# Kernel tuning notes

Hardware: AMD Instinct MI355X
Metric: run time of the kernel (lower is better)

The kernel has to match this reference:

```python
import jax, jax.numpy as jnp
import numpy as np

B, C, H, W, K = 2, 36, 512, 512, 9
GROUPS, GSIZE = 3, 12  # channel groups 0:12, 12:24, 24:36


def _grid_sample_bilinear(feat, gx, gy):
    """Bilinear grid_sample, align_corners=True. feat [B,C,H,W]; gx,gy [B,H,W] in [-1,1]."""
    Bn, Cn, Hn, Wn = feat.shape
    px = (gx + 1.0) * 0.5 * (Wn - 1)
    py = (gy + 1.0) * 0.5 * (Hn - 1)
    x0 = jnp.floor(px)
    y0 = jnp.floor(py)
    wx = (px - x0)[:, None, :, :]
    wy = (py - y0)[:, None, :, :]
    x0i = jnp.clip(x0.astype(jnp.int32), 0, Wn - 1)
    x1i = jnp.clip(x0i + 1, 0, Wn - 1)
    y0i = jnp.clip(y0.astype(jnp.int32), 0, Hn - 1)
    y1i = jnpip = jnp.clip(y0.astype(jnp.int32) + 1, 0, Hn - 1)
    flat = feat.reshape(Bn, Cn, Hn * Wn)
    gather = jax.vmap(lambda f, yi, xi: f[:, yi * Wn + xi])  # -> [B,C,H,W]
    v00 = gather(flat, y0i, x0i)
    v01 = gather(flat, y0i, x1i)
    v10 = gather(flat, y1i, x0i)
    v11 = gather(flat, y1i, x1i)
    return (v00 * (1 - wx) * (1 - wy) + v01 * wx * (1 - wy)
            + v10 * (1 - wx) * wy + v11 * wx * wy)


def setup_inputs() -> dict:
    key = jax.random.key(0)
    k1, k2, k3 = jax.random.split(key, 3)
    features = jax.random.normal(k1, (B, C, H, W), jnp.float32)
    offset_x = jax.random.normal(k2, (B, K, H, W), jnp.float32) * 16.0
    offset_y = jax.random.normal(k3, (B, K, H, W), jnp.float32) * 16.0
    left_x = jnp.broadcast_to(jnp.arange(W, dtype=jnp.float32)[None, None, None, :], (B, 1, H, W))
    left_y = jnp.broadcast_to(jnp.arange(H, dtype=jnp.float32)[None, None, :, None], (B, 1, H, W))
    return {"features": features, "offset_x": offset_x, "offset_y": offset_y,
            "left_x": jnp.array(left_x), "left_y": jnp.array(left_y)}


def reference(features, offset_x, offset_y, left_x, left_y):
    Hn, Wn = features.shape[2], features.shape[3]
    # clamp candidate coords to image, then normalize to [-1,1]
    rx = jnp.clip(left_x + offset_x, 0.0, Wn - 1)
    ry = jnp.clip(left_y + offset_y, 0.0, Hn - 1)
    gx = (rx - (Wn - 1) / 2.0) / ((Wn - 1) / 2.0)  # [B,K,H,W]
    gy = (ry - (Hn - 1) / 2.0) / ((Hn - 1) / 2.0)

    def per_candidate(g):
        gxk, gyk = g  # each [B,H,W]
        a = _grid_sample_bilinear(features, gxk, gyk)  # [B,36,H,W]
        a2 = jnp.roll(a, 12, axis=1)
        a3 = jnp.roll(a, 24, axis=1)

        def grp_mean(d):  # [B,36,H,W] -> [B,3,H,W] mean over 12-channel groups
            return d.reshape(d.shape[0], GROUPS, GSIZE, d.shape[2], d.shape[3]).mean(axis=2)

        s = jnp.concatenate([grp_mean(-jnp.abs(features - a)),
                             grp_mean(-jnp.abs(features - a2)),
                             grp_mean(-jnp.abs(features - a3))], axis=1)  # [B,9,H,W]
        return jnp.max(s, axis=1)  # top-1 of sort == max  -> [B,H,W]

    strengths = jax.lax.map(per_candidate,
                            (jnp.moveaxis(gx, 1, 0), jnp.moveaxis(gy, 1, 0)))  # [K,B,H,W]
    strengths = jnp.moveaxis(strengths, 0, 1)  # [B,K,H,W]

    wgt = jax.nn.softmax(strengths * 1000.0, axis=1)
    ox = jnp.sum(offset_x * wgt, axis=1, keepdims=True)
    oy = jnp.sum(offset_y * wgt, axis=1, keepdims=True)
    oy = jnp.clip(oy + left_y, 0.0, Hn - 1) - left_y
    ox = jnp.clip(ox + left_x, 0.0, Wn - 1) - left_x
    return ox, oy
```

## Files before the change

kernel.cpp:

```cpp
#include <hip/hip_runtime.h>
#include <math.h>

#define B_ 2
#define C_ 36
#define H_ 512
#define W_ 512
#define K_ 9
#define HW_ (H_ * W_)
#define ROWF4 (W_ * C_ / 4)

__global__ __launch_bounds__(256) void transpose_kernel(const float* __restrict__ in,
                                                        float* __restrict__ out) {
  __shared__ float tile[64][37];
  int blk = blockIdx.x;
  int wt = blk & 7;
  int h = (blk >> 3) & (H_ - 1);
  int b = blk >> 12;
  int w0 = wt << 6;
  int tid = threadIdx.x;
  const float* src = in + ((size_t)b * C_) * HW_ + (size_t)h * W_ + w0;
#pragma unroll
  for (int it = 0; it < 9; ++it) {
    int idx = it * 256 + tid;
    int c = idx >> 6;
    int wl = idx & 63;
    tile[wl][c] = src[(size_t)c * HW_ + wl];
  }
  __syncthreads();
  float* dst = out + (((size_t)b * H_ + h) * W_ + w0) * C_;
#pragma unroll
  for (int it = 0; it < 9; ++it) {
    int idx = it * 256 + tid;
    int wl = idx / 36;
    int c = idx - wl * 36;
    dst[idx] = tile[wl][c];
  }
}

__global__ __launch_bounds__(64, 4) void eval_kernel_cw(const float* __restrict__ feat,
                                                        const float* __restrict__ offx,
                                                        const float* __restrict__ offy,
                                                        float* __restrict__ out) {
  __shared__ __align__(16) float scratch[64 * 36];
  __shared__ __align__(16) float4 w_lds[64];
  __shared__ int a_lds[64];

  int tid = threadIdx.x;
  int blk = blockIdx.x;
  int region = blk & 7;
  int slot = blk >> 3;
  int b = region >> 2;
  int qd = region & 3;
  int qy = (qd >> 1) << 8;
  int qx = (qd & 1) << 8;
  int tr = slot >> 5;
  int tc = slot & 31;
  if (tr & 1) tc = 31 - tc;
  int h = qy + tr * 8 + (tid >> 3);
  int w = qx + tc * 8 + (tid & 7);
  int ph = h * W_ + w;
  int p = b * HW_ + ph;

  const float4* feat4 = reinterpret_cast<const float4*>(feat);

  float F[C_];
  {
    const float4* myF = feat4 + (size_t)p * 9;
#pragma unroll
    for (int i = 0; i < 9; ++i) {
      float4 v = myF[i];
      F[4 * i + 0] = v.x; F[4 * i + 1] = v.y; F[4 * i + 2] = v.z; F[4 * i + 3] = v.w;
    }
  }

  int g = tid / 9;
  int q = tid - 9 * g;

  float lx = (float)w;
  float ly = (float)h;
  const float* oxb = offx + (size_t)b * K_ * HW_ + ph;
  const float* oyb = offy + (size_t)b * K_ * HW_ + ph;

  float M = -INFINITY, den = 0.f, axs = 0.f, ays = 0.f;

#pragma unroll 1
  for (int k = 0; k < K_; ++k) {
    float ox = oxb[k * HW_];
    float oy = oyb[k * HW_];
    float rx = fminf(fmaxf(lx + ox, 0.0f), 511.0f);
    float ry = fminf(fmaxf(ly + oy, 0.0f), 511.0f);
    float gx = (rx - 255.5f) / 255.5f;
    float gy = (ry - 255.5f) / 255.5f;
    float px = (gx + 1.0f) * 0.5f * 511.0f;
    float py = (gy + 1.0f) * 0.5f * 511.0f;
    int x0 = (int)floorf(px); x0 = (x0 > 510) ? 510 : x0;
    int y0 = (int)floorf(py); y0 = (y0 > 510) ? 510 : y0;
    float wx = px - (float)x0;
    float wy = py - (float)y0;
    w_lds[tid] = make_float4((1.0f - wx) * (1.0f - wy), wx * (1.0f - wy),
                             (1.0f - wx) * wy, wx * wy);
    a_lds[tid] = ((b * H_ + y0) * W_ + x0) * 9;
    __syncthreads();

    int tt = g;
#pragma unroll 1
    for (int r = 0; r < 10; ++r) {
      int t = (tt > 63) ? 63 : tt;
      int tb = a_lds[t];
      float4 W4 = w_lds[t];
      const float4* r0 = feat4 + tb;
      float4 v00 = r0[q];
      float4 v01 = r0[9 + q];
      float4 v10 = r0[ROWF4 + q];
      float4 v11 = r0[ROWF4 + 9 + q];
      float4 a4;
      a4.x = W4.x * v00.x + W4.y * v01.x + W4.z * v10.x + W4.w * v11.x;
      a4.y = W4.x * v00.y + W4.y * v01.y + W4.z * v10.y + W4.w * v11.y;
      a4.z = W4.x * v00.z + W4.y * v01.z + W4.z * v10.z + W4.w * v11.z;
      a4.w = W4.x * v00.w + W4.y * v01.w + W4.z * v10.w + W4.w * v11.w;
      if (tt < 64 && tid < 63) {
        *reinterpret_cast<float4*>(&scratch[t * 36 + 4 * q]) = a4;
      }
      tt += 7;
    }
    __syncthreads();

    float D[9] = {0.f, 0.f, 0.f, 0.f, 0.f, 0.f, 0.f, 0.f, 0.f};
    const float4* sc = reinterpret_cast<const float4*>(&scratch[tid * 36]);
#pragma unroll
    for (int q2 = 0; q2 < 9; ++q2) {
      float4 a4 = sc[q2];
      float av[4] = {a4.x, a4.y, a4.z, a4.w};
      int ga = q2 / 3;
      int f0 = 4 * (q2 % 3);
#pragma unroll
      for (int j = 0; j < 4; ++j) {
        D[ga]     += fabsf(F[f0 + j]      - av[j]);
        D[3 + ga] += fabsf(F[12 + f0 + j] - av[j]);
        D[6 + ga] += fabsf(F[24 + f0 + j] - av[j]);
      }
    }
    float mn = D[0];
#pragma unroll
    for (int j = 1; j < 9; ++j) mn = fminf(mn, D[j]);
    float xk = -(mn / 12.0f) * 1000.0f;

    float nm = fmaxf(M, xk);
    float scl = expf(M - nm);
    float ek = expf(xk - nm);
    den = den * scl + ek;
    axs = axs * scl + ox * ek;
    ays = ays * scl + oy * ek;
    M = nm;
  }

  float resx = axs / den;
  float resy = ays / den;
  out[p] = fminf(fmaxf(resx + lx, 0.0f), 511.0f) - lx;
  out[B_ * HW_ + p] = fminf(fmaxf(resy + ly, 0.0f), 511.0f) - ly;
}

__global__ __launch_bounds__(256) void eval_kernel_n(const float* __restrict__ feat,
                                                     const float* __restrict__ offx,
                                                     const float* __restrict__ offy,
                                                     float* __restrict__ out) {
  int p = blockIdx.x * 256 + threadIdx.x;
  int ph = p & (HW_ - 1);
  int b = p >> 18;
  float F[C_];
  const float* fb = feat + (size_t)b * C_ * HW_ + ph;
#pragma unroll
  for (int c = 0; c < C_; ++c) F[c] = fb[(size_t)c * HW_];
  float lx = (float)(ph & (W_ - 1));
  float ly = (float)((ph >> 9) & (H_ - 1));
  const float* oxb = offx + (size_t)b * K_ * HW_ + ph;
  const float* oyb = offy + (size_t)b * K_ * HW_ + ph;
  float M = -INFINITY, den = 0.f, ax = 0.f, ay = 0.f;
#pragma unroll 1
  for (int k = 0; k < K_; ++k) {
    float ox = oxb[k * HW_];
    float oy = oyb[k * HW_];
    float rx = fminf(fmaxf(lx + ox, 0.0f), 511.0f);
    float ry = fminf(fmaxf(ly + oy, 0.0f), 511.0f);
    float gx = (rx - 255.5f) / 255.5f;
    float gy = (ry - 255.5f) / 255.5f;
    float px = (gx + 1.0f) * 0.5f * 511.0f;
    float py = (gy + 1.0f) * 0.5f * 511.0f;
    int x0 = (int)floorf(px); x0 = (x0 > 510) ? 510 : x0;
    int y0 = (int)floorf(py); y0 = (y0 > 510) ? 510 : y0;
    float wx = px - (float)x0;
    float wy = py - (float)y0;
    float w00 = (1.0f - wx) * (1.0f - wy);
    float w01 = wx * (1.0f - wy);
    float w10 = (1.0f - wx) * wy;
    float w11 = wx * wy;
    float D[9] = {0.f, 0.f, 0.f, 0.f, 0.f, 0.f, 0.f, 0.f, 0.f};
    const float* pl = feat + (size_t)b * C_ * HW_ + (size_t)y0 * W_ + x0;
#pragma unroll
    for (int c = 0; c < C_; ++c) {
      const float* q0 = pl + (size_t)c * HW_;
      float v00 = q0[0], v01 = q0[1];
      float v10 = q0[W_], v11 = q0[W_ + 1];
      float a = v00 * w00 + v01 * w01 + v10 * w10 + v11 * w11;
      int i = c % 12;
      int ga = c / 12;
      D[ga]     += fabsf(F[i]      - a);
      D[3 + ga] += fabsf(F[12 + i] - a);
      D[6 + ga] += fabsf(F[24 + i] - a);
    }
    float mn = D[0];
#pragma unroll
    for (int j = 1; j < 9; ++j) mn = fminf(mn, D[j]);
    float xk = -(mn / 12.0f) * 1000.0f;
    float nm = fmaxf(M, xk);
    float sc = expf(M - nm);
    float ek = expf(xk - nm);
    den = den * sc + ek;
    ax = ax * sc + ox * ek;
    ay = ay * sc + oy * ek;
    M = nm;
  }
  float resx = ax / den;
  float resy = ay / den;
  out[p] = fminf(fmaxf(resx + lx, 0.0f), 511.0f) - lx;
  out[B_ * HW_ + p] = fminf(fmaxf(resy + ly, 0.0f), 511.0f) - ly;
}

extern "C" void kernel_launch(void* const* d_in, const int* in_sizes, int n_in,
                              void* d_out, int out_size, void* d_ws, size_t ws_size,
                              hipStream_t stream) {
  const float* features = (const float*)d_in[0];
  const float* offset_x = (const float*)d_in[1];
  const float* offset_y = (const float*)d_in[2];
  float* out = (float*)d_out;

  const int npix = B_ * HW_;
  const size_t need = (size_t)npix * C_ * sizeof(float);

  if (ws_size >= need) {
    float* featT = (float*)d_ws;
    transpose_kernel<<<B_ * H_ * (W_ / 64), 256, 0, stream>>>(features, featT);
    eval_kernel_cw<<<npix / 64, 64, 0, stream>>>(featT, offset_x, offset_y, out);
  } else {
    eval_kernel_n<<<npix / 256, 256, 0, stream>>>(features, offset_x, offset_y, out);
  }
}
```

Before: 342.0 us.

## Prefetch offsets and software-pipeline bilinear gather loads in eval kernel

Preloads all nine candidate offsets per pixel into registers before the candidate loop. It also restructures the gather loop as a fully unrolled five-deep register pipeline, so that up to twenty float4 gather loads are in flight per thread. To make room for the extra registers, the launch-bounds occupancy hint is lowered from 4 to 2. The goal is to hide gather latency through memory-level parallelism, at the cost of fewer resident waves and higher register pressure.

After: 321.4 us. -6.0%, faster.

```diff
diff --git a/kernel.cpp b/kernel.cpp
--- a/kernel.cpp
+++ b/kernel.cpp
@@ -37,7 +37,7 @@
   }
 }
 
-__global__ __launch_bounds__(64, 4) void eval_kernel_cw(const float* __restrict__ feat,
+__global__ __launch_bounds__(64, 2) void eval_kernel_cw(const float* __restrict__ feat,
                                                         const float* __restrict__ offx,
                                                         const float* __restrict__ offy,
                                                         float* __restrict__ out) {
@@ -63,6 +63,15 @@
 
   const float4* feat4 = reinterpret_cast<const float4*>(feat);
 
+  const float* oxb = offx + (size_t)b * K_ * HW_ + ph;
+  const float* oyb = offy + (size_t)b * K_ * HW_ + ph;
+  float oxv[K_], oyv[K_];
+#pragma unroll
+  for (int k = 0; k < K_; ++k) {
+    oxv[k] = oxb[k * HW_];
+    oyv[k] = oyb[k * HW_];
+  }
+
   float F[C_];
   {
     const float4* myF = feat4 + (size_t)p * 9;
@@ -78,15 +87,13 @@
 
   float lx = (float)w;
   float ly = (float)h;
-  const float* oxb = offx + (size_t)b * K_ * HW_ + ph;
-  const float* oyb = offy + (size_t)b * K_ * HW_ + ph;
 
   float M = -INFINITY, den = 0.f, axs = 0.f, ays = 0.f;
 
 #pragma unroll 1
   for (int k = 0; k < K_; ++k) {
-    float ox = oxb[k * HW_];
-    float oy = oyb[k * HW_];
+    float ox = oxv[k];
+    float oy = oyv[k];
     float rx = fminf(fmaxf(lx + ox, 0.0f), 511.0f);
     float ry = fminf(fmaxf(ly + oy, 0.0f), 511.0f);
     float gx = (rx - 255.5f) / 255.5f;
@@ -102,17 +109,24 @@
     a_lds[tid] = ((b * H_ + y0) * W_ + x0) * 9;
     __syncthreads();
 
-    int tt = g;
-#pragma unroll 1
+    float4 L[5][4];
+#pragma unroll
+    for (int r = 0; r < 5; ++r) {
+      int tt = 7 * r + g;
+      int t = (tt > 63) ? 63 : tt;
+      const float4* r0 = feat4 + a_lds[t];
+      L[r][0] = r0[q];
+      L[r][1] = r0[9 + q];
+      L[r][2] = r0[ROWF4 + q];
+      L[r][3] = r0[ROWF4 + 9 + q];
+    }
+#pragma unroll
     for (int r = 0; r < 10; ++r) {
+      int s = r % 5;
+      int tt = 7 * r + g;
       int t = (tt > 63) ? 63 : tt;
-      int tb = a_lds[t];
       float4 W4 = w_lds[t];
-      const float4* r0 = feat4 + tb;
-      float4 v00 = r0[q];
-      float4 v01 = r0[9 + q];
-      float4 v10 = r0[ROWF4 + q];
-      float4 v11 = r0[ROWF4 + 9 + q];
+      float4 v00 = L[s][0], v01 = L[s][1], v10 = L[s][2], v11 = L[s][3];
       float4 a4;
       a4.x = W4.x * v00.x + W4.y * v01.x + W4.z * v10.x + W4.w * v11.x;
       a4.y = W4.x * v00.y + W4.y * v01.y + W4.z * v10.y + W4.w * v11.y;
@@ -121,7 +135,15 @@
       if (tt < 64 && tid < 63) {
         *reinterpret_cast<float4*>(&scratch[t * 36 + 4 * q]) = a4;
       }
-      tt += 7;
+      if (r + 5 < 10) {
+        int tt2 = 7 * (r + 5) + g;
+        int t2 = (tt2 > 63) ? 63 : tt2;
+        const float4* r0 = feat4 + a_lds[t2];
+        L[s][0] = r0[q];
+        L[s][1] = r0[9 + q];
+        L[s][2] = r0[ROWF4 + q];
+        L[s][3] = r0[ROWF4 + 9 + q];
+      }
     }
     __syncthreads();
 
```
